# Performance work log

Measured on AMD Instinct MI355X. Metric: run time of the kernel, lower is better.

The kernel has to match this reference:

```python
import jax, jax.numpy as jnp
import numpy as np

VOL_LO = np.array([-40.0, -40.0, -1.0], np.float32)
VOL_HI = np.array([40.0, 40.0, 5.4], np.float32)
VOXEL = 0.4
GRID = (200, 200, 16)  # ((hi-lo)/voxel).int() as in __init__
NUM_CLASSES = 18
EMPTY_LABEL = 17
K = 10  # static per-gaussian tile: 6*sigma_max/VOXEL + 1 <= 10 since sigma <= 0.5
EPS = 1e-6
N_GAUSS = 8192


def quat_to_rotmat(q):
    # wxyz quaternion -> rotation matrix (normalized, as in 3DGS)
    q = q / jnp.linalg.norm(q, axis=-1, keepdims=True)
    w, x, y, z = q[..., 0], q[..., 1], q[..., 2], q[..., 3]
    R = jnp.stack([
        1 - 2 * (y * y + z * z), 2 * (x * y - w * z), 2 * (x * z + w * y),
        2 * (x * y + w * z), 1 - 2 * (x * x + z * z), 2 * (y * z - w * x),
        2 * (x * z - w * y), 2 * (y * z + w * x), 1 - 2 * (x * x + y * y),
    ], axis=-1)
    return R.reshape(q.shape[:-1] + (3, 3))


def _grid_coords():
    H, W, D = GRID
    ii, jj, kk = jnp.meshgrid(jnp.arange(H), jnp.arange(W), jnp.arange(D), indexing='ij')
    g = jnp.stack([ii, jj, kk], axis=-1).astype(jnp.float32) + 0.5  # voxel centers
    return g * VOXEL + jnp.asarray(VOL_LO)


def setup_inputs() -> dict:
    key = jax.random.key(0)
    k1, k2, k3, k4, k5 = jax.random.split(key, 5)
    lo = jnp.asarray(VOL_LO)
    hi = jnp.asarray(VOL_HI)
    means3d = jax.random.uniform(k1, (N_GAUSS, 3)) * (hi - lo) + lo
    opacities = jax.random.uniform(k2, (N_GAUSS, 1))
    features = jax.random.normal(k3, (N_GAUSS, NUM_CLASSES - 1))
    scales = jax.random.uniform(k4, (N_GAUSS, 3)) * 0.4 + 0.1  # sigma in [0.1, 0.5]
    rotations = jax.random.normal(k5, (N_GAUSS, 4))
    empty_scalar = jnp.full((1,), 10.0, jnp.float32)
    return {"means3d": means3d, "opacities": opacities, "features": features,
            "scales": scales, "rotations": rotations, "empty_scalar": empty_scalar}


def reference(means3d, opacities, features, scales, rotations, empty_scalar):
    H, W, D = GRID
    lo = jnp.asarray(VOL_LO)
    hi = jnp.asarray(VOL_HI)
    dims = jnp.array(GRID, jnp.int32)

    # covariances = (R diag(s)) (R diag(s))^T
    R = quat_to_rotmat(rotations)                 # [N,3,3]
    Lm = R * scales[:, None, :]
    cov = Lm @ jnp.swapaxes(Lm, -1, -2)           # [N,3,3]
    cov_inv = jnp.linalg.inv(cov)
    sig = jnp.sqrt(jnp.diagonal(cov, axis1=-2, axis2=-1))  # [N,3]

    # clamped 3-sigma bounds + skip test (strict, matching torch)
    b_lo = jnp.clip(means3d - 3.0 * sig, lo, hi)
    b_hi = jnp.clip(means3d + 3.0 * sig, lo, hi)
    valid = (((b_lo > lo) | (b_hi > lo)) & ((b_lo < hi) | (b_hi < hi))).all(-1)  # [N]
    i_lo = ((b_lo - lo) / VOXEL).astype(jnp.int32)
    i_hi = ((b_hi - lo) / VOXEL).astype(jnp.int32)

    # static KxKxK tile per gaussian, masked to the inclusive [i_lo, i_hi] slice
    o = jnp.arange(K, dtype=jnp.int32)
    oi, oj, ok = jnp.meshgrid(o, o, o, indexing='ij')
    offs = jnp.stack([oi, oj, ok], -1).reshape(-1, 3)          # [K3,3]
    vox = i_lo[:, None, :] + offs[None]                        # [N,K3,3]
    mask = (vox <= i_hi[:, None, :]).all(-1) & (vox < dims).all(-1) & valid[:, None]

    coords = (vox.astype(jnp.float32) + 0.5) * VOXEL + lo      # voxel centers
    diff = coords - means3d[:, None, :]                        # [N,K3,3]
    maha = jnp.einsum('nki,nij,nkj->nk', diff, cov_inv, diff)  # [N,K3]
    dens = jnp.where(mask, opacities * jnp.exp(-0.5 * maha), 0.0)

    flat = jnp.where(mask, vox[..., 0] * (W * D) + vox[..., 1] * D + vox[..., 2], 0)

    feat18 = jnp.concatenate([features, jnp.zeros_like(features[:, :1])], -1)  # [N,18]
    gd = jnp.zeros((H * W * D,), jnp.float32).at[flat.reshape(-1)].add(dens.reshape(-1))
    gf = jnp.zeros((H * W * D, NUM_CLASSES), jnp.float32).at[flat.reshape(-1)].add(
        (dens[..., None] * feat18[:, None, :]).reshape(-1, NUM_CLASSES))

    # appended 'empty' gaussian spans the full grid -> splat densely
    gc = _grid_coords()                                        # [H,W,D,3]
    e_mean = (lo + hi) / 2.0
    e_range = hi - lo
    e_inv = jnp.diag(1.0 / (e_range ** 2))
    de = gc - e_mean
    maha_e = jnp.einsum('hwdi,ij,hwdj->hwd', de, e_inv, de)
    dens_e = jnp.exp(-0.5 * maha_e)                            # empty opacity = 1
    e_feat = jnp.zeros((NUM_CLASSES,), jnp.float32).at[EMPTY_LABEL].add(empty_scalar[0])

    grid_density = gd.reshape(H, W, D) + dens_e
    grid_feats = gf.reshape(H, W, D, NUM_CLASSES) + dens_e[..., None] * e_feat
    grid_feats = grid_feats / jnp.maximum(grid_density[..., None], EPS)
    return grid_density[..., None], grid_feats
```

## Files before the change

kernel.cpp:

```cpp
#include <hip/hip_runtime.h>

namespace {
constexpr int GH = 200, GW = 200, GD = 16;
constexpr int NV = GH * GW * GD;
constexpr int NCLS = 18;
constexpr int NF = 17;
constexpr int NG = 8192;
constexpr int KMAX = 10;
constexpr float VOX = 0.4f;
constexpr float LO0 = -40.f, LO1 = -40.f, LO2 = -1.f;
constexpr float HI0 = 40.f, HI1 = 40.f, HI2 = 5.4f;
constexpr float EPSV = 1e-6f;

constexpr int TILE_XY = 4;
constexpr int NTX = GH / TILE_XY;
constexpr int NTY = GW / TILE_XY;
constexpr int NT = NTX * NTY;
constexpr int REC_DW = 32;
constexpr int REC_V4 = REC_DW / 4;
constexpr int CAP = 128;
constexpr int CH = 32;

constexpr float NHL2E = -0.72134752044448170368f;
}

__global__ __launch_bounds__(64) void gv_bin(
    const float* __restrict__ means,
    const float* __restrict__ opac,
    const float* __restrict__ feats,
    const float* __restrict__ scales,
    const float* __restrict__ rots,
    int* __restrict__ counts,
    float4* __restrict__ lists)
{
    const int g = blockIdx.x * blockDim.x + threadIdx.x;
    if (g >= NG) return;

    const float mx = means[g * 3 + 0];
    const float my = means[g * 3 + 1];
    const float mz = means[g * 3 + 2];
    const float sx = scales[g * 3 + 0];
    const float sy = scales[g * 3 + 1];
    const float sz = scales[g * 3 + 2];
    float qw = rots[g * 4 + 0];
    float qx = rots[g * 4 + 1];
    float qy = rots[g * 4 + 2];
    float qz = rots[g * 4 + 3];

    const float qn = rsqrtf(qw * qw + qx * qx + qy * qy + qz * qz);
    qw *= qn; qx *= qn; qy *= qn; qz *= qn;
    const float r00 = 1.f - 2.f * (qy * qy + qz * qz);
    const float r01 = 2.f * (qx * qy - qw * qz);
    const float r02 = 2.f * (qx * qz + qw * qy);
    const float r10 = 2.f * (qx * qy + qw * qz);
    const float r11 = 1.f - 2.f * (qx * qx + qz * qz);
    const float r12 = 2.f * (qy * qz - qw * qx);
    const float r20 = 2.f * (qx * qz - qw * qy);
    const float r21 = 2.f * (qy * qz + qw * qx);
    const float r22 = 1.f - 2.f * (qx * qx + qy * qy);

    const float s0 = sx * sx, s1 = sy * sy, s2 = sz * sz;
    const float c00 = r00 * r00 * s0 + r01 * r01 * s1 + r02 * r02 * s2;
    const float c11 = r10 * r10 * s0 + r11 * r11 * s1 + r12 * r12 * s2;
    const float c22 = r20 * r20 * s0 + r21 * r21 * s1 + r22 * r22 * s2;
    const float i0 = 1.f / s0, i1 = 1.f / s1, i2 = 1.f / s2;
    const float a00 = r00 * r00 * i0 + r01 * r01 * i1 + r02 * r02 * i2;
    const float a01 = r00 * r10 * i0 + r01 * r11 * i1 + r02 * r12 * i2;
    const float a02 = r00 * r20 * i0 + r01 * r21 * i1 + r02 * r22 * i2;
    const float a11 = r10 * r10 * i0 + r11 * r11 * i1 + r12 * r12 * i2;
    const float a12 = r10 * r20 * i0 + r11 * r21 * i1 + r12 * r22 * i2;
    const float a22 = r20 * r20 * i0 + r21 * r21 * i1 + r22 * r22 * i2;

    const float m3[3] = { mx, my, mz };
    const float sg[3] = { sqrtf(c00), sqrtf(c11), sqrtf(c22) };
    const float lo3[3] = { LO0, LO1, LO2 };
    const float hi3[3] = { HI0, HI1, HI2 };
    const int dims[3] = { GH, GW, GD };

    int il[3], sp[3];
    bool valid = true;
#pragma unroll
    for (int ax = 0; ax < 3; ++ax) {
        const float bl = fminf(fmaxf(m3[ax] - 3.f * sg[ax], lo3[ax]), hi3[ax]);
        const float bh = fminf(fmaxf(m3[ax] + 3.f * sg[ax], lo3[ax]), hi3[ax]);
        valid = valid &&
                (((bl > lo3[ax]) || (bh > lo3[ax])) && ((bl < hi3[ax]) || (bh < hi3[ax])));
        const int a = (int)((bl - lo3[ax]) / VOX);
        const int b = (int)((bh - lo3[ax]) / VOX);
        int s = b - a + 1;
        s = min(s, KMAX);
        s = min(s, dims[ax] - a);
        s = max(s, 0);
        il[ax] = a;
        sp[ax] = s;
    }

    if (!valid || sp[0] <= 0 || sp[1] <= 0 || sp[2] <= 0) return;
    const int pack = sp[0] | (sp[1] << 8) | (sp[2] << 16);

    const float* F = feats + (size_t)g * NF;
    float4 R[REC_V4];
    R[0] = make_float4(mx, my, mz, opac[g]);
    R[1] = make_float4(NHL2E * a00, NHL2E * a11, NHL2E * a22, 2.f * NHL2E * a01);
    R[2] = make_float4(2.f * NHL2E * a02, 2.f * NHL2E * a12, F[0], F[1]);
    R[3] = make_float4(F[2], F[3], F[4], F[5]);
    R[4] = make_float4(F[6], F[7], F[8], F[9]);
    R[5] = make_float4(F[10], F[11], F[12], F[13]);
    R[6] = make_float4(F[14], F[15], F[16], __int_as_float(il[0]));
    R[7] = make_float4(__int_as_float(il[1]), __int_as_float(il[2]),
                       __int_as_float(pack), 0.f);

    const int tx0 = il[0] / TILE_XY;
    const int tx1 = (il[0] + sp[0] - 1) / TILE_XY;
    const int ty0 = il[1] / TILE_XY;
    const int ty1 = (il[1] + sp[1] - 1) / TILE_XY;
    for (int tx = tx0; tx <= tx1; ++tx)
        for (int ty = ty0; ty <= ty1; ++ty) {
            const int tile = tx * NTY + ty;
            const int idx = atomicAdd(counts + tile, 1);
            if (idx < CAP) {
                float4* dst = lists + ((size_t)tile * CAP + idx) * REC_V4;
#pragma unroll
                for (int u = 0; u < REC_V4; ++u) dst[u] = R[u];
            }
        }
}

__global__ __launch_bounds__(64) void gv_gather(
    const int* __restrict__ counts,
    const float4* __restrict__ lists,
    const float* __restrict__ empty_scalar,
    float* __restrict__ out)
{
    __shared__ float4 s_rec[2][CH * REC_V4];

    const int tile = blockIdx.x;
    const int tx = tile / NTY;
    const int ty = tile - tx * NTY;

    const int lane = threadIdx.x;
    const int lx = lane >> 4;
    const int ly = (lane >> 2) & 3;
    const int vz0 = (lane & 3) << 2;

    const int vx = tx * TILE_XY + lx;
    const int vy = ty * TILE_XY + ly;
    const float cx = ((float)vx + 0.5f) * VOX + LO0;
    const float cy = ((float)vy + 0.5f) * VOX + LO1;

    const int n = min(counts[tile], CAP);
    const float4* __restrict__ tl = lists + (size_t)tile * CAP * REC_V4;

    float accd[4] = { 0.f, 0.f, 0.f, 0.f };
    float accf[4][NF];
#pragma unroll
    for (int j = 0; j < 4; ++j)
#pragma unroll
        for (int c = 0; c < NF; ++c) accf[j][c] = 0.f;

    const int e_ld = lane >> 1;
    const int q_ld = lane & 1;
    float4 r0, r1, r2, r3;

    const int nchunk = (n + CH - 1) / CH;
    int buf = 0;

    if (nchunk > 0 && e_ld < n) {
        const float4* src = tl + (size_t)e_ld * REC_V4 + q_ld * 4;
        r0 = src[0]; r1 = src[1]; r2 = src[2]; r3 = src[3];
        float4* dst = &s_rec[0][e_ld * REC_V4 + q_ld * 4];
        dst[0] = r0; dst[1] = r1; dst[2] = r2; dst[3] = r3;
    }
    __syncthreads();

    for (int c = 0; c < nchunk; ++c) {
        const int nidx = (c + 1) * CH + e_ld;
        const bool nact = (c + 1 < nchunk) && (nidx < n);
        if (nact) {
            const float4* src = tl + (size_t)nidx * REC_V4 + q_ld * 4;
            r0 = src[0]; r1 = src[1]; r2 = src[2]; r3 = src[3];
        }

        const int m = min(CH, n - c * CH);
        for (int e = 0; e < m; ++e) {
            const float4* E = &s_rec[buf][e * REC_V4];
            const float4 e0 = E[0], e1 = E[1], e2 = E[2], e3 = E[3];
            const float4 e4 = E[4], e5 = E[5], e6 = E[6], e7 = E[7];

            const int il0 = __float_as_int(e6.w);
            const int il1 = __float_as_int(e7.x);
            const int il2 = __float_as_int(e7.y);
            const int pk  = __float_as_int(e7.z);

            const bool inxy =
                ((unsigned)(vx - il0) < (unsigned)(pk & 255)) &
                ((unsigned)(vy - il1) < (unsigned)((pk >> 8) & 255));
            const unsigned spz = (unsigned)((pk >> 16) & 255);

            const float dx = cx - e0.x;
            const float dy = cy - e0.y;
            const float q0 = e1.x * dx * dx + e1.y * dy * dy + e1.w * dx * dy;
            const float q1 = e2.x * dx + e2.y * dy;
            const float A22 = e1.z;
            const float op = e0.w, mzv = e0.z;

            const float f[NF] = { e2.z, e2.w, e3.x, e3.y, e3.z, e3.w,
                                  e4.x, e4.y, e4.z, e4.w,
                                  e5.x, e5.y, e5.z, e5.w,
                                  e6.x, e6.y, e6.z };

#pragma unroll
            for (int j = 0; j < 4; ++j) {
                const float cz = ((float)(vz0 + j) + 0.5f) * VOX + LO2;
                const float dz = cz - mzv;
                const float ee = q0 + dz * (q1 + A22 * dz);
                const bool in = inxy & ((unsigned)(vz0 + j - il2) < spz);
                const float dens = op * __builtin_amdgcn_exp2f(ee);
                if (in) {
                    accd[j] += dens;
#pragma unroll
                    for (int cc = 0; cc < NF; ++cc) accf[j][cc] += dens * f[cc];
                }
            }
        }

        if (nact) {
            float4* dst = &s_rec[buf ^ 1][e_ld * REC_V4 + q_ld * 4];
            dst[0] = r0; dst[1] = r1; dst[2] = r2; dst[3] = r3;
        }
        __syncthreads();
        buf ^= 1;
    }

    const float es = empty_scalar[0];
    const float ex = (cx - 0.5f * (LO0 + HI0)) / (HI0 - LO0);
    const float ey = (cy - 0.5f * (LO1 + HI1)) / (HI1 - LO1);
    const float exy = ex * ex + ey * ey;

    float dsv[4], dev[4];
#pragma unroll
    for (int j = 0; j < 4; ++j) {
        const float cz = ((float)(vz0 + j) + 0.5f) * VOX + LO2;
        const float ez = (cz - 0.5f * (LO2 + HI2)) / (HI2 - LO2);
        dev[j] = __expf(-0.5f * (exy + ez * ez));
        dsv[j] = accd[j] + dev[j];
    }

    const int vbase = (vx * GW + vy) * GD + vz0;
    *(float4*)(out + vbase) = make_float4(dsv[0], dsv[1], dsv[2], dsv[3]);

#pragma unroll
    for (int j = 0; j < 4; ++j) {
        const float inv = 1.f / fmaxf(dsv[j], EPSV);
        float vals[NCLS];
#pragma unroll
        for (int c = 0; c < NF; ++c) vals[c] = accf[j][c] * inv;
        vals[NF] = dev[j] * es * inv;
        float2* of2 = (float2*)(out + NV + (size_t)(vbase + j) * NCLS);
#pragma unroll
        for (int p = 0; p < NCLS / 2; ++p)
            of2[p] = make_float2(vals[2 * p], vals[2 * p + 1]);
    }
}

extern "C" void kernel_launch(void* const* d_in, const int* in_sizes, int n_in,
                              void* d_out, int out_size, void* d_ws, size_t ws_size,
                              hipStream_t stream) {
    const float* means  = (const float*)d_in[0];
    const float* opac   = (const float*)d_in[1];
    const float* feats  = (const float*)d_in[2];
    const float* scales = (const float*)d_in[3];
    const float* rots   = (const float*)d_in[4];
    const float* esc    = (const float*)d_in[5];

    int*    counts = (int*)d_ws;
    float4* lists  = (float4*)((char*)d_ws + 64 * 1024);

    hipMemsetAsync(counts, 0, sizeof(int) * NT, stream);

    gv_bin<<<NG / 64, 64, 0, stream>>>(means, opac, feats, scales, rots,
                                       counts, lists);
    gv_gather<<<NT, 64, 0, stream>>>(counts, lists, esc, (float*)d_out);
}
```

Baseline: 105.1 us.

## Map one voxel per thread in gather with 256-thread blocks and wave-level skip

The gather kernel now uses 256 threads per tile, one voxel each, where before it used 64 threads handling 4 z-voxels apiece. This cuts per-thread accumulator registers from 4x18 to 18, which should raise occupancy and thread-level parallelism. Each gaussian record's bounds are checked first, and the wavefront skips the rest of the record load and exp when no lane is inside. Costs are more blocks' worth of shared-memory broadcast reads per record and scalar instead of float4 density stores.

```diff
diff --git a/kernel.cpp b/kernel.cpp
--- a/kernel.cpp
+++ b/kernel.cpp
@@ -126,7 +126,7 @@
         }
 }
 
-__global__ __launch_bounds__(64) void gv_gather(
+__global__ __launch_bounds__(256) void gv_gather(
     const int* __restrict__ counts,
     const float4* __restrict__ lists,
     const float* __restrict__ empty_scalar,
@@ -138,95 +138,83 @@
     const int tx = tile / NTY;
     const int ty = tile - tx * NTY;
 
-    const int lane = threadIdx.x;
-    const int lx = lane >> 4;
-    const int ly = (lane >> 2) & 3;
-    const int vz0 = (lane & 3) << 2;
+    const int t = threadIdx.x;
+    const int vz = t & 15;
+    const int ly = (t >> 4) & 3;
+    const int lx = t >> 6;
 
     const int vx = tx * TILE_XY + lx;
     const int vy = ty * TILE_XY + ly;
     const float cx = ((float)vx + 0.5f) * VOX + LO0;
     const float cy = ((float)vy + 0.5f) * VOX + LO1;
+    const float cz = ((float)vz + 0.5f) * VOX + LO2;
 
     const int n = min(counts[tile], CAP);
     const float4* __restrict__ tl = lists + (size_t)tile * CAP * REC_V4;
 
-    float accd[4] = { 0.f, 0.f, 0.f, 0.f };
-    float accf[4][NF];
-#pragma unroll
-    for (int j = 0; j < 4; ++j)
-#pragma unroll
-        for (int c = 0; c < NF; ++c) accf[j][c] = 0.f;
-
-    const int e_ld = lane >> 1;
-    const int q_ld = lane & 1;
-    float4 r0, r1, r2, r3;
+    float accd = 0.f;
+    float accf[NF];
+#pragma unroll
+    for (int c = 0; c < NF; ++c) accf[c] = 0.f;
+
+    const int e_ld = t >> 3;
+    const int q_ld = t & 7;
+    float4 r;
 
     const int nchunk = (n + CH - 1) / CH;
     int buf = 0;
 
     if (nchunk > 0 && e_ld < n) {
-        const float4* src = tl + (size_t)e_ld * REC_V4 + q_ld * 4;
-        r0 = src[0]; r1 = src[1]; r2 = src[2]; r3 = src[3];
-        float4* dst = &s_rec[0][e_ld * REC_V4 + q_ld * 4];
-        dst[0] = r0; dst[1] = r1; dst[2] = r2; dst[3] = r3;
+        s_rec[0][e_ld * REC_V4 + q_ld] = tl[(size_t)e_ld * REC_V4 + q_ld];
     }
     __syncthreads();
 
     for (int c = 0; c < nchunk; ++c) {
         const int nidx = (c + 1) * CH + e_ld;
         const bool nact = (c + 1 < nchunk) && (nidx < n);
-        if (nact) {
-            const float4* src = tl + (size_t)nidx * REC_V4 + q_ld * 4;
-            r0 = src[0]; r1 = src[1]; r2 = src[2]; r3 = src[3];
-        }
+        if (nact) r = tl[(size_t)nidx * REC_V4 + q_ld];
 
         const int m = min(CH, n - c * CH);
         for (int e = 0; e < m; ++e) {
             const float4* E = &s_rec[buf][e * REC_V4];
-            const float4 e0 = E[0], e1 = E[1], e2 = E[2], e3 = E[3];
-            const float4 e4 = E[4], e5 = E[5], e6 = E[6], e7 = E[7];
+            const float4 e6 = E[6], e7 = E[7];
 
             const int il0 = __float_as_int(e6.w);
             const int il1 = __float_as_int(e7.x);
             const int il2 = __float_as_int(e7.y);
             const int pk  = __float_as_int(e7.z);
 
-            const bool inxy =
+            const bool in =
                 ((unsigned)(vx - il0) < (unsigned)(pk & 255)) &
-                ((unsigned)(vy - il1) < (unsigned)((pk >> 8) & 255));
-            const unsigned spz = (unsigned)((pk >> 16) & 255);
+                ((unsigned)(vy - il1) < (unsigned)((pk >> 8) & 255)) &
+                ((unsigned)(vz - il2) < (unsigned)((pk >> 16) & 255));
+
+            if (!__any(in)) continue;
+
+            const float4 e0 = E[0], e1 = E[1], e2 = E[2], e3 = E[3];
+            const float4 e4 = E[4], e5 = E[5];
 
             const float dx = cx - e0.x;
             const float dy = cy - e0.y;
+            const float dz = cz - e0.z;
             const float q0 = e1.x * dx * dx + e1.y * dy * dy + e1.w * dx * dy;
             const float q1 = e2.x * dx + e2.y * dy;
-            const float A22 = e1.z;
-            const float op = e0.w, mzv = e0.z;
-
-            const float f[NF] = { e2.z, e2.w, e3.x, e3.y, e3.z, e3.w,
-                                  e4.x, e4.y, e4.z, e4.w,
-                                  e5.x, e5.y, e5.z, e5.w,
-                                  e6.x, e6.y, e6.z };
-
-#pragma unroll
-            for (int j = 0; j < 4; ++j) {
-                const float cz = ((float)(vz0 + j) + 0.5f) * VOX + LO2;
-                const float dz = cz - mzv;
-                const float ee = q0 + dz * (q1 + A22 * dz);
-                const bool in = inxy & ((unsigned)(vz0 + j - il2) < spz);
-                const float dens = op * __builtin_amdgcn_exp2f(ee);
-                if (in) {
-                    accd[j] += dens;
-#pragma unroll
-                    for (int cc = 0; cc < NF; ++cc) accf[j][cc] += dens * f[cc];
-                }
+            const float ee = q0 + dz * (q1 + e1.z * dz);
+            const float dens = e0.w * __builtin_amdgcn_exp2f(ee);
+
+            if (in) {
+                accd += dens;
+                const float f[NF] = { e2.z, e2.w, e3.x, e3.y, e3.z, e3.w,
+                                      e4.x, e4.y, e4.z, e4.w,
+                                      e5.x, e5.y, e5.z, e5.w,
+                                      e6.x, e6.y, e6.z };
+#pragma unroll
+                for (int cc = 0; cc < NF; ++cc) accf[cc] += dens * f[cc];
             }
         }
 
         if (nact) {
-            float4* dst = &s_rec[buf ^ 1][e_ld * REC_V4 + q_ld * 4];
-            dst[0] = r0; dst[1] = r1; dst[2] = r2; dst[3] = r3;
+            s_rec[buf ^ 1][e_ld * REC_V4 + q_ld] = r;
         }
         __syncthreads();
         buf ^= 1;
@@ -235,32 +223,23 @@
     const float es = empty_scalar[0];
     const float ex = (cx - 0.5f * (LO0 + HI0)) / (HI0 - LO0);
     const float ey = (cy - 0.5f * (LO1 + HI1)) / (HI1 - LO1);
-    const float exy = ex * ex + ey * ey;
-
-    float dsv[4], dev[4];
-#pragma unroll
-    for (int j = 0; j < 4; ++j) {
-        const float cz = ((float)(vz0 + j) + 0.5f) * VOX + LO2;
-        const float ez = (cz - 0.5f * (LO2 + HI2)) / (HI2 - LO2);
-        dev[j] = __expf(-0.5f * (exy + ez * ez));
-        dsv[j] = accd[j] + dev[j];
-    }
-
-    const int vbase = (vx * GW + vy) * GD + vz0;
-    *(float4*)(out + vbase) = make_float4(dsv[0], dsv[1], dsv[2], dsv[3]);
-
-#pragma unroll
-    for (int j = 0; j < 4; ++j) {
-        const float inv = 1.f / fmaxf(dsv[j], EPSV);
-        float vals[NCLS];
-#pragma unroll
-        for (int c = 0; c < NF; ++c) vals[c] = accf[j][c] * inv;
-        vals[NF] = dev[j] * es * inv;
-        float2* of2 = (float2*)(out + NV + (size_t)(vbase + j) * NCLS);
-#pragma unroll
-        for (int p = 0; p < NCLS / 2; ++p)
-            of2[p] = make_float2(vals[2 * p], vals[2 * p + 1]);
-    }
+    const float ez = (cz - 0.5f * (LO2 + HI2)) / (HI2 - LO2);
+    const float dev = __expf(-0.5f * (ex * ex + ey * ey + ez * ez));
+    const float dsv = accd + dev;
+
+    const int vidx = (vx * GW + vy) * GD + vz;
+    out[vidx] = dsv;
+
+    const float inv = 1.f / fmaxf(dsv, EPSV);
+    float vals[NCLS];
+#pragma unroll
+    for (int c = 0; c < NF; ++c) vals[c] = accf[c] * inv;
+    vals[NF] = dev * es * inv;
+
+    float2* of2 = (float2*)(out + NV + (size_t)vidx * NCLS);
+#pragma unroll
+    for (int p = 0; p < NCLS / 2; ++p)
+        of2[p] = make_float2(vals[2 * p], vals[2 * p + 1]);
 }
 
 extern "C" void kernel_launch(void* const* d_in, const int* in_sizes, int n_in,
@@ -280,5 +259,5 @@
 
     gv_bin<<<NG / 64, 64, 0, stream>>>(means, opac, feats, scales, rots,
                                        counts, lists);
-    gv_gather<<<NT, 64, 0, stream>>>(counts, lists, esc, (float*)d_out);
-}
+    gv_gather<<<NT, 256, 0, stream>>>(counts, lists, esc, (float*)d_out);
+}
```

New measurement: 111.1 us. 5.7% more time.
